# Optimization experiments

Measured on AMD Instinct MI355X. Metric: run time of the kernel, lower is better.

Reference implementation:

```python
import jax, jax.numpy as jnp
import numpy as np

B, S, DIM = 2, 2048, 2048
H, KV = 16, 8
HD = DIM // H          # 128 head_dim
N_REP = H // KV        # 2


def _rope(x, cos, sin):
    # x: (B,S,h,HD) with interleaved (real, imag) pairs along last dim
    xr = x[..., 0::2]                      # (B,S,h,HD/2)
    xi = x[..., 1::2]
    cos = cos[None, :, None, :]            # (1,S,1,HD/2)
    sin = sin[None, :, None, :]
    or_ = xr * cos - xi * sin
    oi_ = xr * sin + xi * cos
    return jnp.stack([or_, oi_], axis=-1).reshape(x.shape)


def setup_inputs() -> dict:
    key = jax.random.key(0)
    ks = jax.random.split(key, 5)
    x = jax.random.normal(ks[0], (B, S, DIM), dtype=jnp.float32)
    # RoPE tables: theta = 10000, half = HD/2
    inv_freq = 1.0 / (10000.0 ** (np.arange(0, HD, 2, dtype=np.float32) / HD))
    t = np.arange(S, dtype=np.float32)
    ang = np.outer(t, inv_freq)                           # (S, HD/2)
    freqs_cos = jnp.asarray(np.cos(ang), dtype=jnp.float32)
    freqs_sin = jnp.asarray(np.sin(ang), dtype=jnp.float32)
    sc = 0.02
    wq = jax.random.normal(ks[1], (DIM, H * HD), dtype=jnp.float32) * sc
    wk = jax.random.normal(ks[2], (DIM, KV * HD), dtype=jnp.float32) * sc
    wv = jax.random.normal(ks[3], (DIM, KV * HD), dtype=jnp.float32) * sc
    wo = jax.random.normal(ks[4], (DIM, DIM), dtype=jnp.float32) * sc
    return {"x": x, "freqs_cos": freqs_cos, "freqs_sin": freqs_sin,
            "wq": wq, "wk": wk, "wv": wv, "wo": wo}


def reference(x, freqs_cos, freqs_sin, wq, wk, wv, wo):
    b, s, _ = x.shape
    xq = (x @ wq).reshape(b, s, H, HD)
    xk = (x @ wk).reshape(b, s, KV, HD)
    xv = (x @ wv).reshape(b, s, KV, HD)
    xq = _rope(xq, freqs_cos, freqs_sin)
    xk = _rope(xk, freqs_cos, freqs_sin)
    # GQA: repeat kv heads n_rep times along head axis
    xk = jnp.repeat(xk, N_REP, axis=2)     # (b,s,H,HD)
    xv = jnp.repeat(xv, N_REP, axis=2)
    scores = jnp.einsum('bqhd,bkhd->bhqk', xq, xk) / jnp.sqrt(
        jnp.asarray(HD, dtype=x.dtype))
    mask = jnp.triu(jnp.full((s, s), -jnp.inf, dtype=x.dtype), k=1)
    attn = jax.nn.softmax(scores + mask[None, None, :, :], axis=-1)
    out = jnp.einsum('bhqk,bkhd->bqhd', attn, xv).reshape(b, s, DIM)
    return out @ wo
```

## Files before the change

### kernel.cpp

```cpp
#include <hip/hip_runtime.h>

typedef unsigned short u16;
typedef short bf16x8 __attribute__((ext_vector_type(8)));
typedef float f32x4 __attribute__((ext_vector_type(4)));
typedef float f32x16 __attribute__((ext_vector_type(16)));
typedef int i32x2 __attribute__((ext_vector_type(2)));
typedef unsigned int u32x4 __attribute__((ext_vector_type(4)));
typedef unsigned short u16x4 __attribute__((ext_vector_type(4)));
typedef unsigned short u16x8 __attribute__((ext_vector_type(8)));

#define S_LEN 2048
#define NHEAD 16
#define NKV 8
#define HD 128

__device__ __forceinline__ u16 f2bf(float f) {
  unsigned u = __builtin_bit_cast(unsigned, f);
  u = (u + 0x7FFFu + ((u >> 16) & 1u)) >> 16;
  return (u16)u;
}
__device__ __forceinline__ float bf2f(u16 h) {
  unsigned u = ((unsigned)h) << 16;
  return __builtin_bit_cast(float, u);
}

__device__ __forceinline__ void gl_lds16(const void* g, void* l) {
  __builtin_amdgcn_global_load_lds(
      (const __attribute__((address_space(1))) unsigned int*)g,
      (__attribute__((address_space(3))) unsigned int*)l, 16, 0, 0);
}

__device__ __forceinline__ unsigned cvtpk_bf16(float a, float b) {
  unsigned r;
  asm("v_cvt_pk_bf16_f32 %0, %1, %2" : "=v"(r) : "v"(a), "v"(b));
  return r;
}

__global__ __launch_bounds__(256) void conv_bf16(const float* __restrict__ in,
                                                 u16* __restrict__ out, int n4) {
  int i = blockIdx.x * 256 + threadIdx.x;
  if (i >= n4) return;
  f32x4 v = *(const f32x4*)(in + (size_t)i * 4);
  u16x4 o;
#pragma unroll
  for (int j = 0; j < 4; ++j) o[j] = f2bf(v[j]);
  *(u16x4*)(out + (size_t)i * 4) = o;
}

__global__ __launch_bounds__(256) void transpose_w4(
    const float* __restrict__ wq, const float* __restrict__ wk,
    const float* __restrict__ wv, const float* __restrict__ wo,
    u16* __restrict__ wcatT, u16* __restrict__ woT) {
  __shared__ float tile[64][65];
  int id = blockIdx.x;
  const float* in;
  u16* out;
  int N, roff, nx;
  if (id < 1024) {
    in = wq; out = wcatT; N = 2048; roff = 0; nx = 32;
  } else if (id < 1536) {
    in = wk; out = wcatT; N = 1024; roff = 2048; nx = 16; id -= 1024;
  } else if (id < 2048) {
    in = wv; out = wcatT; N = 1024; roff = 3072; nx = 16; id -= 1536;
  } else {
    in = wo; out = woT; N = 2048; roff = 0; nx = 32; id -= 2048;
  }
  int bx = id % nx;
  int by = id / nx;
  int k0 = by * 64, n0 = bx * 64;
  int tx = threadIdx.x & 63, ty = threadIdx.x >> 6;
#pragma unroll
  for (int p = 0; p < 16; ++p) {
    int r = p * 4 + ty;
    tile[r][tx] = in[(size_t)(k0 + r) * N + n0 + tx];
  }
  __syncthreads();
#pragma unroll
  for (int p = 0; p < 16; ++p) {
    int r = p * 4 + ty;
    out[(size_t)(roff + n0 + r) * 2048 + k0 + tx] = f2bf(tile[tx][r]);
  }
}

__global__ __launch_bounds__(256) void rope_qk(u16* __restrict__ q, u16* __restrict__ k,
                                               const float* __restrict__ fc,
                                               const float* __restrict__ fs) {
  const int QC = 2 * NHEAD * S_LEN * HD / 8;
  const int KC = 2 * NKV * S_LEN * HD / 8;
  int i = blockIdx.x * 256 + threadIdx.x;
  if (i >= QC + KC) return;
  u16* base;
  float scale;
  size_t e;
  if (i < QC) {
    base = q;
    e = (size_t)i * 8;
    scale = 0.12751744540368598f;
  } else {
    base = k;
    e = (size_t)(i - QC) * 8;
    scale = 1.0f;
  }
  int d8 = (int)(e & 127);
  int s = (int)((e >> 7) & (S_LEN - 1));
  int dp0 = d8 >> 1;
  u16x8 v = *(const u16x8*)(base + e);
  u16x8 o;
#pragma unroll
  for (int p = 0; p < 4; ++p) {
    float xr = bf2f(v[2 * p]), xi = bf2f(v[2 * p + 1]);
    float c = fc[s * 64 + dp0 + p], sn = fs[s * 64 + dp0 + p];
    o[2 * p] = f2bf((xr * c - xi * sn) * scale);
    o[2 * p + 1] = f2bf((xr * sn + xi * c) * scale);
  }
  *(u16x8*)(base + e) = o;
}

template <int EPI>
__global__ __launch_bounds__(512, 1) void gemm3r(
    const u16* __restrict__ A, const u16* __restrict__ Bt, float* __restrict__ Cf,
    u16* __restrict__ Qo, u16* __restrict__ Ko, u16* __restrict__ Vo, int N, int ntn) {
  constexpr int K = 2048, NT = K / 64;
  constexpr int BSZ = (128 + 256) * 64;
  __shared__ __align__(16) u16 lds[3][BSZ];

  const int t = threadIdx.x;
  const int l = t & 63, lh = l >> 4, ll = l & 15;
  const int w = t >> 6, wm = w >> 2, wn = w & 3;

  const int bid = blockIdx.x;
  const int swz = (bid & 7) * (gridDim.x >> 3) + (bid >> 3);
  const int tm = swz / ntn, tn = swz % ntn;

  const u16* Ab = A + (size_t)tm * 128 * K;
  const u16* Bb = Bt + (size_t)tn * 256 * K;

  const int sr = t >> 3;
  const int sc8 = ((t & 7) ^ (sr & 7)) * 8;

  f32x4 acc[4][4] = {};

  auto STAGE = [&](int tau) {
    const int kt = tau * 64;
    u16* buf = &lds[tau % 3][0];
#pragma unroll
    for (int c = 0; c < 2; ++c)
      gl_lds16(Ab + (size_t)(c * 64 + sr) * K + kt + sc8, buf + c * 4096 + t * 8);
#pragma unroll
    for (int c = 0; c < 4; ++c)
      gl_lds16(Bb + (size_t)(c * 64 + sr) * K + kt + sc8,
               buf + 8192 + c * 4096 + t * 8);
  };

  STAGE(0);
  STAGE(1);
  __builtin_amdgcn_s_waitcnt(0xF70 | 6);
  __builtin_amdgcn_s_barrier();
  asm volatile("" ::: "memory");

  for (int tt = 0; tt < NT; ++tt) {
    if (tt + 2 < NT) STAGE(tt + 2);
    const u16* bufA = &lds[tt % 3][0];
    const u16* bufB = bufA + 8192;
#pragma unroll
    for (int kk = 0; kk < 2; ++kk) {
      const int cb = ((kk * 4 + lh) ^ (ll & 7)) * 8;
      bf16x8 af[4], bv[4];
#pragma unroll
      for (int m = 0; m < 4; ++m)
        af[m] = *(const bf16x8*)(bufA + (wm * 64 + m * 16 + ll) * 64 + cb);
#pragma unroll
      for (int n = 0; n < 4; ++n)
        bv[n] = *(const bf16x8*)(bufB + (wn * 64 + n * 16 + ll) * 64 + cb);
      __builtin_amdgcn_s_setprio(1);
#pragma unroll
      for (int m = 0; m < 4; ++m)
#pragma unroll
        for (int n = 0; n < 4; ++n)
          acc[m][n] =
              __builtin_amdgcn_mfma_f32_16x16x32_bf16(af[m], bv[n], acc[m][n], 0, 0, 0);
      __builtin_amdgcn_s_setprio(0);
    }
    if (tt + 1 < NT) {
      if (tt + 2 < NT)
        __builtin_amdgcn_s_waitcnt(0xF70 | 6);
      else
        __builtin_amdgcn_s_waitcnt(0xF70);
      __builtin_amdgcn_s_barrier();
      asm volatile("" ::: "memory");
    }
  }

#pragma unroll
  for (int m = 0; m < 4; ++m)
#pragma unroll
    for (int n = 0; n < 4; ++n)
#pragma unroll
      for (int j = 0; j < 4; ++j) {
        int row = tm * 128 + wm * 64 + m * 16 + lh * 4 + j;
        int col = tn * 256 + wn * 64 + n * 16 + ll;
        if constexpr (EPI == 0) {
          Cf[(size_t)row * N + col] = acc[m][n][j];
        } else {
          int b = row >> 11, s = row & (S_LEN - 1);
          u16 val = f2bf(acc[m][n][j]);
          int d = col & 127;
          if (col < 2048) {
            int hh = col >> 7;
            Qo[(((size_t)b * NHEAD + hh) * S_LEN + s) * HD + d] = val;
          } else if (col < 3072) {
            int kh = (col >> 7) & 7;
            Ko[(((size_t)b * NKV + kh) * S_LEN + s) * HD + d] = val;
          } else {
            int kh = (col >> 7) & 7;
            Vo[(((size_t)b * NKV + kh) * S_LEN + s) * HD + d] = val;
          }
        }
      }
}

__global__ __launch_bounds__(256) void transpose_v(const u16* __restrict__ V,
                                                   u16* __restrict__ Vt) {
  __shared__ u16 tile[64][72];
  int id = blockIdx.x;
  int bkv = id >> 6;
  int dt = (id >> 5) & 1;
  int st = id & 31;
  const u16* Vb = V + (size_t)bkv * S_LEN * HD;
  u16* Vo = Vt + (size_t)bkv * HD * S_LEN;
  int r = threadIdx.x >> 3, c8 = (threadIdx.x & 7) * 8;
#pragma unroll
  for (int it = 0; it < 2; ++it) {
    int rr = it * 32 + r;
    *(u16x8*)(&tile[rr][c8]) =
        *(const u16x8*)(Vb + (size_t)(st * 64 + rr) * HD + dt * 64 + c8);
  }
  __syncthreads();
#pragma unroll
  for (int it = 0; it < 2; ++it) {
    int rr = it * 32 + r;
    u16x8 o;
#pragma unroll
    for (int j = 0; j < 8; ++j) o[j] = tile[c8 + j][rr];
    *(u16x8*)(Vo + (size_t)(dt * 64 + rr) * S_LEN + st * 64 + c8) = o;
  }
}

__global__ __launch_bounds__(256, 2) void attn_fwd(const u16* __restrict__ Q,
                                                   const u16* __restrict__ Kh,
                                                   const u16* __restrict__ Vt,
                                                   u16* __restrict__ O) {
  __shared__ __align__(16) u16 KS[2][64 * 128];
  __shared__ __align__(16) u16 VS[2][128 * 64];

  const int t = threadIdx.x;
  const int l = t & 63, hi = l >> 5, ll = l & 31;
  const int wq = t >> 6;

  const int bid = blockIdx.x;
  const int qt = 15 - (bid >> 5);
  const int bh = bid & 31;
  const int b = bh >> 4, h = bh & 15;
  const int bkv = b * NKV + (h >> 1);

  const u16* Qb = Q + (size_t)bh * S_LEN * HD;
  const u16* Kb = Kh + (size_t)bkv * S_LEN * HD;
  const u16* Vb = Vt + (size_t)bkv * HD * S_LEN;

  const int q0w = qt * 128 + wq * 32;
  const int qg = q0w + ll;

  bf16x8 qf[8];
#pragma unroll
  for (int c = 0; c < 8; ++c)
    qf[c] = *(const bf16x8*)(Qb + (size_t)qg * HD + c * 16 + hi * 8);

  const int krow = t >> 4, kslot = t & 15;
  const int vrow = t >> 3, vslot = t & 7;
  u16x8 krg[4], vrg[4];

  auto loadKV = [&](int tile) {
    const int kv0 = tile * 64;
#pragma unroll
    for (int c = 0; c < 4; ++c) {
      int r = c * 16 + krow;
      int sg = (kslot & 8) | ((kslot & 7) ^ (r & 7));
      krg[c] = *(const u16x8*)(Kb + (size_t)(kv0 + r) * HD + sg * 8);
    }
#pragma unroll
    for (int c = 0; c < 4; ++c) {
      int d = c * 32 + vrow;
      int sg = vslot ^ (d & 7);
      vrg[c] = *(const u16x8*)(Vb + (size_t)d * S_LEN + kv0 + sg * 8);
    }
  };
  auto storeKV = [&](int bi) {
#pragma unroll
    for (int c = 0; c < 4; ++c)
      *(u16x8*)(&KS[bi][(c * 16 + krow) * 128 + kslot * 8]) = krg[c];
#pragma unroll
    for (int c = 0; c < 4; ++c)
      *(u16x8*)(&VS[bi][(c * 32 + vrow) * 64 + vslot * 8]) = vrg[c];
  };

  f32x16 accO[4] = {};
  float m = -1e30f, lsum = 0.f;

  const int nt = 2 * qt + 2;
  loadKV(0);
  storeKV(0);
  __syncthreads();

  for (int tt = 0; tt < nt; ++tt) {
    const int kv0 = tt * 64;
    const bool actn = (tt + 1 < nt);
    if (actn) loadKV(tt + 1);

    if (kv0 <= q0w + 31) {
      const u16* ks = &KS[tt & 1][0];
      const u16* vs = &VS[tt & 1][0];

      f32x16 st[2] = {};
      __builtin_amdgcn_s_setprio(1);
#pragma unroll
      for (int c = 0; c < 8; ++c) {
        int slot = 2 * c + hi;
        int eff = (slot & 8) | ((slot & 7) ^ (ll & 7));
        bf16x8 kf0 = *(const bf16x8*)(ks + (size_t)ll * 128 + eff * 8);
        st[0] = __builtin_amdgcn_mfma_f32_32x32x16_bf16(kf0, qf[c], st[0], 0, 0, 0);
        bf16x8 kf1 = *(const bf16x8*)(ks + (size_t)(32 + ll) * 128 + eff * 8);
        st[1] = __builtin_amdgcn_mfma_f32_32x32x16_bf16(kf1, qf[c], st[1], 0, 0, 0);
      }
      __builtin_amdgcn_s_setprio(0);

      if (kv0 + 63 > q0w) {
#pragma unroll
        for (int f = 0; f < 2; ++f)
#pragma unroll
          for (int r = 0; r < 16; ++r) {
            int kvg = kv0 + f * 32 + (r & 3) + 8 * (r >> 2) + 4 * hi;
            if (kvg > qg) st[f][r] = -1e30f;
          }
      }

      float a[16];
#pragma unroll
      for (int i = 0; i < 16; ++i) a[i] = fmaxf(st[0][i], st[1][i]);
#pragma unroll
      for (int s = 8; s >= 1; s >>= 1)
#pragma unroll
        for (int i = 0; i < 8; ++i)
          if (i < s) a[i] = fmaxf(a[i], a[i + s]);
      float pmax = fmaxf(a[0], __shfl_xor(a[0], 32));

      if (tt == 0) {
        m = pmax;
      } else if (!__all(pmax <= m + 8.0f)) {
        float mnew = fmaxf(m, pmax);
        float corr = __builtin_amdgcn_exp2f(m - mnew);
        m = mnew;
        lsum *= corr;
        int ci = __builtin_bit_cast(int, corr);
#pragma unroll
        for (int reg = 0; reg < 16; ++reg) {
          int row = (reg & 3) + 8 * (reg >> 2) + 4 * hi;
          float cq = __builtin_bit_cast(
              float, __builtin_amdgcn_ds_bpermute(row << 2, ci));
#pragma unroll
          for (int dblk = 0; dblk < 4; ++dblk) accO[dblk][reg] *= cq;
        }
      }

#pragma unroll
      for (int f = 0; f < 2; ++f)
#pragma unroll
        for (int r = 0; r < 16; ++r)
          st[f][r] = __builtin_amdgcn_exp2f(st[f][r] - m);
      float s1[16];
#pragma unroll
      for (int i = 0; i < 16; ++i) s1[i] = st[0][i] + st[1][i];
#pragma unroll
      for (int s = 8; s >= 1; s >>= 1)
#pragma unroll
        for (int i = 0; i < 8; ++i)
          if (i < s) s1[i] += s1[i + s];
      lsum += s1[0];

      unsigned pk[8][2];
#pragma unroll
      for (int bg = 0; bg < 8; ++bg)
#pragma unroll
        for (int ap = 0; ap < 2; ++ap)
          pk[bg][ap] = cvtpk_bf16(st[bg >> 2][(bg & 3) * 4 + 2 * ap],
                                  st[bg >> 2][(bg & 3) * 4 + 2 * ap + 1]);

      __builtin_amdgcn_s_setprio(1);
#pragma unroll
      for (int kc = 0; kc < 4; ++kc) {
        i32x2 sa = __builtin_amdgcn_permlane32_swap(
            (int)pk[2 * kc][0], (int)pk[2 * kc + 1][0], false, false);
        i32x2 sb = __builtin_amdgcn_permlane32_swap(
            (int)pk[2 * kc][1], (int)pk[2 * kc + 1][1], false, false);
        union {
          unsigned u[4];
          bf16x8 v;
        } pa;
        pa.u[0] = (unsigned)sa[0];
        pa.u[1] = (unsigned)sb[0];
        pa.u[2] = (unsigned)sa[1];
        pa.u[3] = (unsigned)sb[1];
        int eff = (2 * kc + hi) ^ (ll & 7);
#pragma unroll
        for (int dblk = 0; dblk < 4; ++dblk) {
          bf16x8 vf = *(const bf16x8*)(vs + (size_t)(dblk * 32 + ll) * 64 + eff * 8);
          accO[dblk] =
              __builtin_amdgcn_mfma_f32_32x32x16_bf16(pa.v, vf, accO[dblk], 0, 0, 0);
        }
      }
      __builtin_amdgcn_s_setprio(0);
    }

    __syncthreads();
    if (actn) storeKV((tt + 1) & 1);
    __syncthreads();
  }

  lsum += __shfl_xor(lsum, 32);
  float linv = 1.0f / lsum;
  int li = __builtin_bit_cast(int, linv);
  float inv[16];
#pragma unroll
  for (int reg = 0; reg < 16; ++reg) {
    int row = (reg & 3) + 8 * (reg >> 2) + 4 * hi;
    inv[reg] = __builtin_bit_cast(float, __builtin_amdgcn_ds_bpermute(row << 2, li));
  }
#pragma unroll
  for (int dblk = 0; dblk < 4; ++dblk)
#pragma unroll
    for (int reg = 0; reg < 16; ++reg) {
      int row = (reg & 3) + 8 * (reg >> 2) + 4 * hi;
      O[(size_t)(b * S_LEN + q0w + row) * 2048 + h * HD + dblk * 32 + ll] =
          f2bf(accO[dblk][reg] * inv[reg]);
    }
}

extern "C" void kernel_launch(void* const* d_in, const int* in_sizes, int n_in,
                              void* d_out, int out_size, void* d_ws, size_t ws_size,
                              hipStream_t stream) {
  (void)in_sizes;
  (void)n_in;
  (void)out_size;
  (void)ws_size;
  const float* x = (const float*)d_in[0];
  const float* fc = (const float*)d_in[1];
  const float* fs = (const float*)d_in[2];
  const float* wq = (const float*)d_in[3];
  const float* wk = (const float*)d_in[4];
  const float* wv = (const float*)d_in[5];
  const float* wo = (const float*)d_in[6];
  float* out = (float*)d_out;

  char* ws = (char*)d_ws;
  u16* wcatT = (u16*)ws;
  u16* vtb = (u16*)ws;
  u16* woT = (u16*)(ws + 16777216);
  u16* xo = (u16*)(ws + 25165824);
  u16* qb = (u16*)(ws + 41943040);
  u16* kb = (u16*)(ws + 58720256);
  u16* vb = (u16*)(ws + 67108864);

  conv_bf16<<<8192, 256, 0, stream>>>(x, xo, 2097152);
  transpose_w4<<<3072, 256, 0, stream>>>(wq, wk, wv, wo, wcatT, woT);

  gemm3r<1><<<512, 512, 0, stream>>>(xo, wcatT, nullptr, qb, kb, vb, 4096, 16);
  transpose_v<<<1024, 256, 0, stream>>>(vb, vtb);
  rope_qk<<<6144, 256, 0, stream>>>(qb, kb, fc, fs);
  attn_fwd<<<512, 256, 0, stream>>>(qb, kb, vtb, xo);
  gemm3r<0><<<256, 512, 0, stream>>>(xo, woT, out, nullptr, nullptr, nullptr, 2048, 8);
}
```

Baseline: 212.3 us.

## Enlarge GEMM tiles to 256x256 with 4-stage K=32 LDS pipeline

Replaces the 128x256 GEMM tile and its 3-stage K=64 pipeline with a 256x256 tile that streams K in 32-wide slices through a 4-deep LDS ring. A and B rows share one combined swizzled buffer, and each wave now holds 8x4 accumulators. This raises arithmetic intensity per byte loaded and halves the grid. The cost is fewer blocks: 256 and 128 on a machine with 256 CUs, which leaves part of the GPU idle for the output projection. It also raises register pressure, and the launch bound now asks for 2 blocks per CU.

```diff
diff --git a/kernel.cpp b/kernel.cpp
--- a/kernel.cpp
+++ b/kernel.cpp
@@ -117,12 +117,11 @@
 }
 
 template <int EPI>
-__global__ __launch_bounds__(512, 1) void gemm3r(
+__global__ __launch_bounds__(512, 2) void gemm8p(
     const u16* __restrict__ A, const u16* __restrict__ Bt, float* __restrict__ Cf,
     u16* __restrict__ Qo, u16* __restrict__ Ko, u16* __restrict__ Vo, int N, int ntn) {
-  constexpr int K = 2048, NT = K / 64;
-  constexpr int BSZ = (128 + 256) * 64;
-  __shared__ __align__(16) u16 lds[3][BSZ];
+  constexpr int K = 2048, NH = K / 32;
+  __shared__ __align__(16) u16 lds[4][256 * 64];
 
   const int t = threadIdx.x;
   const int l = t & 63, lh = l >> 4, ll = l & 15;
@@ -132,78 +131,85 @@
   const int swz = (bid & 7) * (gridDim.x >> 3) + (bid >> 3);
   const int tm = swz / ntn, tn = swz % ntn;
 
-  const u16* Ab = A + (size_t)tm * 128 * K;
+  const u16* Ab = A + (size_t)tm * 256 * K;
   const u16* Bb = Bt + (size_t)tn * 256 * K;
 
-  const int sr = t >> 3;
-  const int sc8 = ((t & 7) ^ (sr & 7)) * 8;
-
-  f32x4 acc[4][4] = {};
-
-  auto STAGE = [&](int tau) {
-    const int kt = tau * 64;
-    u16* buf = &lds[tau % 3][0];
-#pragma unroll
-    for (int c = 0; c < 2; ++c)
-      gl_lds16(Ab + (size_t)(c * 64 + sr) * K + kt + sc8, buf + c * 4096 + t * 8);
+  const int srow = t >> 3;
+  const int sphys = t & 7;
+  const int slog = sphys ^ (srow & 7);
+  const u16* sbase = (slog < 4) ? Ab : Bb;
+  const int scol = (slog & 3) * 8;
+
+  f32x4 acc[8][4] = {};
+
+  auto STAGE = [&](int H) {
+    u16* buf = &lds[H & 3][0];
+    const u16* sp = sbase + (size_t)srow * K + H * 32 + scol;
 #pragma unroll
     for (int c = 0; c < 4; ++c)
-      gl_lds16(Bb + (size_t)(c * 64 + sr) * K + kt + sc8,
-               buf + 8192 + c * 4096 + t * 8);
+      gl_lds16(sp + (size_t)c * 64 * K, buf + c * 4096 + t * 8);
+  };
+
+  auto BODY = [&](int H) {
+    const u16* buf = &lds[H & 3][0];
+    bf16x8 af[8], bv[4];
+#pragma unroll
+    for (int i = 0; i < 8; ++i) {
+      int row = wm * 128 + i * 16 + ll;
+      af[i] = *(const bf16x8*)(buf + row * 64 + (lh ^ (ll & 7)) * 8);
+    }
+#pragma unroll
+    for (int n = 0; n < 4; ++n) {
+      int row = wn * 64 + n * 16 + ll;
+      bv[n] = *(const bf16x8*)(buf + row * 64 + ((4 + lh) ^ (ll & 7)) * 8);
+    }
+    __builtin_amdgcn_s_setprio(1);
+#pragma unroll
+    for (int i = 0; i < 8; ++i)
+#pragma unroll
+      for (int n = 0; n < 4; ++n)
+        acc[i][n] =
+            __builtin_amdgcn_mfma_f32_16x16x32_bf16(af[i], bv[n], acc[i][n], 0, 0, 0);
+    __builtin_amdgcn_s_setprio(0);
   };
 
   STAGE(0);
   STAGE(1);
-  __builtin_amdgcn_s_waitcnt(0xF70 | 6);
+  STAGE(2);
+  __builtin_amdgcn_s_waitcnt(0xF70 | 8);
   __builtin_amdgcn_s_barrier();
   asm volatile("" ::: "memory");
 
-  for (int tt = 0; tt < NT; ++tt) {
-    if (tt + 2 < NT) STAGE(tt + 2);
-    const u16* bufA = &lds[tt % 3][0];
-    const u16* bufB = bufA + 8192;
-#pragma unroll
-    for (int kk = 0; kk < 2; ++kk) {
-      const int cb = ((kk * 4 + lh) ^ (ll & 7)) * 8;
-      bf16x8 af[4], bv[4];
-#pragma unroll
-      for (int m = 0; m < 4; ++m)
-        af[m] = *(const bf16x8*)(bufA + (wm * 64 + m * 16 + ll) * 64 + cb);
-#pragma unroll
-      for (int n = 0; n < 4; ++n)
-        bv[n] = *(const bf16x8*)(bufB + (wn * 64 + n * 16 + ll) * 64 + cb);
-      __builtin_amdgcn_s_setprio(1);
-#pragma unroll
-      for (int m = 0; m < 4; ++m)
-#pragma unroll
-        for (int n = 0; n < 4; ++n)
-          acc[m][n] =
-              __builtin_amdgcn_mfma_f32_16x16x32_bf16(af[m], bv[n], acc[m][n], 0, 0, 0);
-      __builtin_amdgcn_s_setprio(0);
-    }
-    if (tt + 1 < NT) {
-      if (tt + 2 < NT)
-        __builtin_amdgcn_s_waitcnt(0xF70 | 6);
-      else
-        __builtin_amdgcn_s_waitcnt(0xF70);
-      __builtin_amdgcn_s_barrier();
-      asm volatile("" ::: "memory");
-    }
-  }
-
-#pragma unroll
-  for (int m = 0; m < 4; ++m)
+  for (int H = 0; H < NH - 3; ++H) {
+    STAGE(H + 3);
+    BODY(H);
+    __builtin_amdgcn_s_waitcnt(0xF70 | 8);
+    __builtin_amdgcn_s_barrier();
+    asm volatile("" ::: "memory");
+  }
+  BODY(NH - 3);
+  __builtin_amdgcn_s_waitcnt(0xF70 | 4);
+  __builtin_amdgcn_s_barrier();
+  asm volatile("" ::: "memory");
+  BODY(NH - 2);
+  __builtin_amdgcn_s_waitcnt(0xF70);
+  __builtin_amdgcn_s_barrier();
+  asm volatile("" ::: "memory");
+  BODY(NH - 1);
+
+#pragma unroll
+  for (int i = 0; i < 8; ++i)
 #pragma unroll
     for (int n = 0; n < 4; ++n)
 #pragma unroll
       for (int j = 0; j < 4; ++j) {
-        int row = tm * 128 + wm * 64 + m * 16 + lh * 4 + j;
+        int row = tm * 256 + wm * 128 + i * 16 + lh * 4 + j;
         int col = tn * 256 + wn * 64 + n * 16 + ll;
         if constexpr (EPI == 0) {
-          Cf[(size_t)row * N + col] = acc[m][n][j];
+          Cf[(size_t)row * N + col] = acc[i][n][j];
         } else {
           int b = row >> 11, s = row & (S_LEN - 1);
-          u16 val = f2bf(acc[m][n][j]);
+          u16 val = f2bf(acc[i][n][j]);
           int d = col & 127;
           if (col < 2048) {
             int hh = col >> 7;
@@ -472,9 +478,9 @@
   conv_bf16<<<8192, 256, 0, stream>>>(x, xo, 2097152);
   transpose_w4<<<3072, 256, 0, stream>>>(wq, wk, wv, wo, wcatT, woT);
 
-  gemm3r<1><<<512, 512, 0, stream>>>(xo, wcatT, nullptr, qb, kb, vb, 4096, 16);
+  gemm8p<1><<<256, 512, 0, stream>>>(xo, wcatT, nullptr, qb, kb, vb, 4096, 16);
   transpose_v<<<1024, 256, 0, stream>>>(vb, vtb);
   rope_qk<<<6144, 256, 0, stream>>>(qb, kb, fc, fs);
   attn_fwd<<<512, 256, 0, stream>>>(qb, kb, vtb, xo);
-  gemm3r<0><<<256, 512, 0, stream>>>(xo, woT, out, nullptr, nullptr, nullptr, 2048, 8);
-}
+  gemm8p<0><<<128, 512, 0, stream>>>(xo, woT, out, nullptr, nullptr, nullptr, 2048, 8);
+}
```

Result: slower. 223.8 us (+5.4%).

## Replace 128x256 GEMM tile with 128x128 tile, 256 threads, BK=32

Applied to the files above, without the earlier changes.

Both GEMMs move from a 128x256 output tile with 512 threads and a K-step of 64 to a 128x128 tile with 256 threads and a K-step of 32. The A and B tiles are interleaved in one shared LDS buffer, with a per-thread XOR swizzle that picks A or B. The grid is doubled so more blocks are in flight, and the smaller LDS and launch-bounds footprint allows more than one block per CU. In exchange, each loaded byte is reused less and there are twice as many barriers per unit of K.

```diff
diff --git a/kernel.cpp b/kernel.cpp
--- a/kernel.cpp
+++ b/kernel.cpp
@@ -117,73 +117,74 @@
 }
 
 template <int EPI>
-__global__ __launch_bounds__(512, 1) void gemm3r(
+__global__ __launch_bounds__(256) void gemm128(
     const u16* __restrict__ A, const u16* __restrict__ Bt, float* __restrict__ Cf,
     u16* __restrict__ Qo, u16* __restrict__ Ko, u16* __restrict__ Vo, int N, int ntn) {
-  constexpr int K = 2048, NT = K / 64;
-  constexpr int BSZ = (128 + 256) * 64;
-  __shared__ __align__(16) u16 lds[3][BSZ];
+  constexpr int K = 2048, NT = K / 32;
+  __shared__ __align__(16) u16 lds[3][128 * 64];
 
   const int t = threadIdx.x;
   const int l = t & 63, lh = l >> 4, ll = l & 15;
-  const int w = t >> 6, wm = w >> 2, wn = w & 3;
+  const int w = t >> 6, wm = w >> 1, wn = w & 1;
 
   const int bid = blockIdx.x;
   const int swz = (bid & 7) * (gridDim.x >> 3) + (bid >> 3);
   const int tm = swz / ntn, tn = swz % ntn;
 
   const u16* Ab = A + (size_t)tm * 128 * K;
-  const u16* Bb = Bt + (size_t)tn * 256 * K;
-
-  const int sr = t >> 3;
-  const int sc8 = ((t & 7) ^ (sr & 7)) * 8;
+  const u16* Bb = Bt + (size_t)tn * 128 * K;
+
+  const int srow = t >> 3;
+  const int sphys = t & 7;
+  const int slog = sphys ^ (srow & 7);
+  const u16* sbase = (slog < 4) ? Ab : Bb;
+  const int scol = (slog & 3) * 8;
 
   f32x4 acc[4][4] = {};
 
-  auto STAGE = [&](int tau) {
-    const int kt = tau * 64;
-    u16* buf = &lds[tau % 3][0];
-#pragma unroll
-    for (int c = 0; c < 2; ++c)
-      gl_lds16(Ab + (size_t)(c * 64 + sr) * K + kt + sc8, buf + c * 4096 + t * 8);
+  auto STAGE = [&](int tt) {
+    u16* buf = &lds[tt % 3][0];
+    const u16* sp = sbase + (size_t)srow * K + tt * 32 + scol;
 #pragma unroll
     for (int c = 0; c < 4; ++c)
-      gl_lds16(Bb + (size_t)(c * 64 + sr) * K + kt + sc8,
-               buf + 8192 + c * 4096 + t * 8);
+      gl_lds16(sp + (size_t)c * 32 * K, buf + c * 2048 + t * 8);
+  };
+
+  auto BODY = [&](int tt) {
+    const u16* buf = &lds[tt % 3][0];
+    bf16x8 af[4], bv[4];
+#pragma unroll
+    for (int m = 0; m < 4; ++m) {
+      int row = wm * 64 + m * 16 + ll;
+      af[m] = *(const bf16x8*)(buf + row * 64 + (lh ^ (ll & 7)) * 8);
+    }
+#pragma unroll
+    for (int n = 0; n < 4; ++n) {
+      int row = wn * 64 + n * 16 + ll;
+      bv[n] = *(const bf16x8*)(buf + row * 64 + ((4 + lh) ^ (ll & 7)) * 8);
+    }
+    __builtin_amdgcn_s_setprio(1);
+#pragma unroll
+    for (int m = 0; m < 4; ++m)
+#pragma unroll
+      for (int n = 0; n < 4; ++n)
+        acc[m][n] =
+            __builtin_amdgcn_mfma_f32_16x16x32_bf16(af[m], bv[n], acc[m][n], 0, 0, 0);
+    __builtin_amdgcn_s_setprio(0);
   };
 
   STAGE(0);
   STAGE(1);
-  __builtin_amdgcn_s_waitcnt(0xF70 | 6);
+  __builtin_amdgcn_s_waitcnt(0xF70 | 4);
   __builtin_amdgcn_s_barrier();
   asm volatile("" ::: "memory");
 
   for (int tt = 0; tt < NT; ++tt) {
     if (tt + 2 < NT) STAGE(tt + 2);
-    const u16* bufA = &lds[tt % 3][0];
-    const u16* bufB = bufA + 8192;
-#pragma unroll
-    for (int kk = 0; kk < 2; ++kk) {
-      const int cb = ((kk * 4 + lh) ^ (ll & 7)) * 8;
-      bf16x8 af[4], bv[4];
-#pragma unroll
-      for (int m = 0; m < 4; ++m)
-        af[m] = *(const bf16x8*)(bufA + (wm * 64 + m * 16 + ll) * 64 + cb);
-#pragma unroll
-      for (int n = 0; n < 4; ++n)
-        bv[n] = *(const bf16x8*)(bufB + (wn * 64 + n * 16 + ll) * 64 + cb);
-      __builtin_amdgcn_s_setprio(1);
-#pragma unroll
-      for (int m = 0; m < 4; ++m)
-#pragma unroll
-        for (int n = 0; n < 4; ++n)
-          acc[m][n] =
-              __builtin_amdgcn_mfma_f32_16x16x32_bf16(af[m], bv[n], acc[m][n], 0, 0, 0);
-      __builtin_amdgcn_s_setprio(0);
-    }
+    BODY(tt);
     if (tt + 1 < NT) {
       if (tt + 2 < NT)
-        __builtin_amdgcn_s_waitcnt(0xF70 | 6);
+        __builtin_amdgcn_s_waitcnt(0xF70 | 4);
       else
         __builtin_amdgcn_s_waitcnt(0xF70);
       __builtin_amdgcn_s_barrier();
@@ -198,7 +199,7 @@
 #pragma unroll
       for (int j = 0; j < 4; ++j) {
         int row = tm * 128 + wm * 64 + m * 16 + lh * 4 + j;
-        int col = tn * 256 + wn * 64 + n * 16 + ll;
+        int col = tn * 128 + wn * 64 + n * 16 + ll;
         if constexpr (EPI == 0) {
           Cf[(size_t)row * N + col] = acc[m][n][j];
         } else {
@@ -472,9 +473,9 @@
   conv_bf16<<<8192, 256, 0, stream>>>(x, xo, 2097152);
   transpose_w4<<<3072, 256, 0, stream>>>(wq, wk, wv, wo, wcatT, woT);
 
-  gemm3r<1><<<512, 512, 0, stream>>>(xo, wcatT, nullptr, qb, kb, vb, 4096, 16);
+  gemm128<1><<<1024, 256, 0, stream>>>(xo, wcatT, nullptr, qb, kb, vb, 4096, 32);
   transpose_v<<<1024, 256, 0, stream>>>(vb, vtb);
   rope_qk<<<6144, 256, 0, stream>>>(qb, kb, fc, fs);
   attn_fwd<<<512, 256, 0, stream>>>(qb, kb, vtb, xo);
-  gemm3r<0><<<256, 512, 0, stream>>>(xo, woT, out, nullptr, nullptr, nullptr, 2048, 8);
-}
+  gemm128<0><<<512, 256, 0, stream>>>(xo, woT, out, nullptr, nullptr, nullptr, 2048, 16);
+}
```

Result: slower. 247.2 us (+16.5%).

## Fuse RoPE and V transpose into QKV GEMM epilogue; split-K output GEMM

Applied to the files above, without the earlier changes.

Applies RoPE (with the query scale) inside the QKV GEMM epilogue, using a lane shuffle to fetch the pair partner. The V tile is transposed through LDS and written straight into the Vt layout, which removes the separate rope_qk and transpose_v kernels and their extra global round trips. The output projection is split along K into two halves over 512 blocks and accumulated with fp32 atomics into an output buffer zeroed beforehand. This fills more CUs, at the cost of atomic traffic, an extra zeroing kernel and order-dependent float summation.

```diff
diff --git a/kernel.cpp b/kernel.cpp
--- a/kernel.cpp
+++ b/kernel.cpp
@@ -45,6 +45,12 @@
 #pragma unroll
   for (int j = 0; j < 4; ++j) o[j] = f2bf(v[j]);
   *(u16x4*)(out + (size_t)i * 4) = o;
+}
+
+__global__ __launch_bounds__(256) void zero_f32(float* __restrict__ p, int n4) {
+  int i = blockIdx.x * 256 + threadIdx.x;
+  if (i >= n4) return;
+  *(f32x4*)(p + (size_t)i * 4) = f32x4{0.f, 0.f, 0.f, 0.f};
 }
 
 __global__ __launch_bounds__(256) void transpose_w4(
@@ -82,45 +88,13 @@
   }
 }
 
-__global__ __launch_bounds__(256) void rope_qk(u16* __restrict__ q, u16* __restrict__ k,
-                                               const float* __restrict__ fc,
-                                               const float* __restrict__ fs) {
-  const int QC = 2 * NHEAD * S_LEN * HD / 8;
-  const int KC = 2 * NKV * S_LEN * HD / 8;
-  int i = blockIdx.x * 256 + threadIdx.x;
-  if (i >= QC + KC) return;
-  u16* base;
-  float scale;
-  size_t e;
-  if (i < QC) {
-    base = q;
-    e = (size_t)i * 8;
-    scale = 0.12751744540368598f;
-  } else {
-    base = k;
-    e = (size_t)(i - QC) * 8;
-    scale = 1.0f;
-  }
-  int d8 = (int)(e & 127);
-  int s = (int)((e >> 7) & (S_LEN - 1));
-  int dp0 = d8 >> 1;
-  u16x8 v = *(const u16x8*)(base + e);
-  u16x8 o;
-#pragma unroll
-  for (int p = 0; p < 4; ++p) {
-    float xr = bf2f(v[2 * p]), xi = bf2f(v[2 * p + 1]);
-    float c = fc[s * 64 + dp0 + p], sn = fs[s * 64 + dp0 + p];
-    o[2 * p] = f2bf((xr * c - xi * sn) * scale);
-    o[2 * p + 1] = f2bf((xr * sn + xi * c) * scale);
-  }
-  *(u16x8*)(base + e) = o;
-}
-
 template <int EPI>
 __global__ __launch_bounds__(512, 1) void gemm3r(
     const u16* __restrict__ A, const u16* __restrict__ Bt, float* __restrict__ Cf,
-    u16* __restrict__ Qo, u16* __restrict__ Ko, u16* __restrict__ Vo, int N, int ntn) {
-  constexpr int K = 2048, NT = K / 64;
+    u16* __restrict__ Qo, u16* __restrict__ Ko, u16* __restrict__ Vt,
+    const float* __restrict__ fc, const float* __restrict__ fs, int N, int ntn) {
+  constexpr int K = 2048;
+  constexpr int NT = (EPI == 1) ? 32 : 16;
   constexpr int BSZ = (128 + 256) * 64;
   __shared__ __align__(16) u16 lds[3][BSZ];
 
@@ -129,11 +103,14 @@
   const int w = t >> 6, wm = w >> 2, wn = w & 3;
 
   const int bid = blockIdx.x;
-  const int swz = (bid & 7) * (gridDim.x >> 3) + (bid >> 3);
+  const int inner = (EPI == 1) ? bid : (bid & 255);
+  const int ngrid = (EPI == 1) ? 512 : 256;
+  const int koff = (EPI == 1) ? 0 : ((bid >> 8) * 1024);
+  const int swz = (inner & 7) * (ngrid >> 3) + (inner >> 3);
   const int tm = swz / ntn, tn = swz % ntn;
 
-  const u16* Ab = A + (size_t)tm * 128 * K;
-  const u16* Bb = Bt + (size_t)tn * 256 * K;
+  const u16* Ab = A + (size_t)tm * 128 * K + koff;
+  const u16* Bb = Bt + (size_t)tn * 256 * K + koff;
 
   const int sr = t >> 3;
   const int sc8 = ((t & 7) ^ (sr & 7)) * 8;
@@ -191,58 +168,68 @@
     }
   }
 
-#pragma unroll
-  for (int m = 0; m < 4; ++m)
-#pragma unroll
-    for (int n = 0; n < 4; ++n)
-#pragma unroll
-      for (int j = 0; j < 4; ++j) {
-        int row = tm * 128 + wm * 64 + m * 16 + lh * 4 + j;
-        int col = tn * 256 + wn * 64 + n * 16 + ll;
-        if constexpr (EPI == 0) {
-          Cf[(size_t)row * N + col] = acc[m][n][j];
-        } else {
-          int b = row >> 11, s = row & (S_LEN - 1);
-          u16 val = f2bf(acc[m][n][j]);
-          int d = col & 127;
-          if (col < 2048) {
-            int hh = col >> 7;
-            Qo[(((size_t)b * NHEAD + hh) * S_LEN + s) * HD + d] = val;
-          } else if (col < 3072) {
-            int kh = (col >> 7) & 7;
-            Ko[(((size_t)b * NKV + kh) * S_LEN + s) * HD + d] = val;
-          } else {
-            int kh = (col >> 7) & 7;
-            Vo[(((size_t)b * NKV + kh) * S_LEN + s) * HD + d] = val;
+  if constexpr (EPI == 0) {
+#pragma unroll
+    for (int m = 0; m < 4; ++m)
+#pragma unroll
+      for (int n = 0; n < 4; ++n)
+#pragma unroll
+        for (int j = 0; j < 4; ++j) {
+          int row = tm * 128 + wm * 64 + m * 16 + lh * 4 + j;
+          int col = tn * 256 + wn * 64 + n * 16 + ll;
+          atomicAdd(&Cf[(size_t)row * N + col], acc[m][n][j]);
+        }
+  } else {
+    if (tn < 12) {
+      const float qsc = 0.12751744540368598f;
+#pragma unroll
+      for (int m = 0; m < 4; ++m)
+#pragma unroll
+        for (int n = 0; n < 4; ++n)
+#pragma unroll
+          for (int j = 0; j < 4; ++j) {
+            int row = tm * 128 + wm * 64 + m * 16 + lh * 4 + j;
+            int col = tn * 256 + wn * 64 + n * 16 + ll;
+            int s = row & (S_LEN - 1), d = col & 127;
+            float v = acc[m][n][j];
+            float p = __shfl_xor(v, 1);
+            int d2 = d >> 1;
+            float c = fc[s * 64 + d2], sn = fs[s * 64 + d2];
+            float r = (d & 1) ? (p * sn + v * c) : (v * c - p * sn);
+            int b = row >> 11;
+            if (tn < 8) {
+              Qo[(((size_t)b * NHEAD + (col >> 7)) * S_LEN + s) * HD + d] =
+                  f2bf(r * qsc);
+            } else {
+              Ko[(((size_t)b * NKV + ((col >> 7) & 7)) * S_LEN + s) * HD + d] =
+                  f2bf(r);
+            }
           }
-        }
-      }
-}
-
-__global__ __launch_bounds__(256) void transpose_v(const u16* __restrict__ V,
-                                                   u16* __restrict__ Vt) {
-  __shared__ u16 tile[64][72];
-  int id = blockIdx.x;
-  int bkv = id >> 6;
-  int dt = (id >> 5) & 1;
-  int st = id & 31;
-  const u16* Vb = V + (size_t)bkv * S_LEN * HD;
-  u16* Vo = Vt + (size_t)bkv * HD * S_LEN;
-  int r = threadIdx.x >> 3, c8 = (threadIdx.x & 7) * 8;
-#pragma unroll
-  for (int it = 0; it < 2; ++it) {
-    int rr = it * 32 + r;
-    *(u16x8*)(&tile[rr][c8]) =
-        *(const u16x8*)(Vb + (size_t)(st * 64 + rr) * HD + dt * 64 + c8);
-  }
-  __syncthreads();
-#pragma unroll
-  for (int it = 0; it < 2; ++it) {
-    int rr = it * 32 + r;
-    u16x8 o;
-#pragma unroll
-    for (int j = 0; j < 8; ++j) o[j] = tile[c8 + j][rr];
-    *(u16x8*)(Vo + (size_t)(dt * 64 + rr) * S_LEN + st * 64 + c8) = o;
+    } else {
+      __syncthreads();
+      u16* vt = (u16*)&lds[0][0];
+#pragma unroll
+      for (int m = 0; m < 4; ++m)
+#pragma unroll
+        for (int n = 0; n < 4; ++n)
+#pragma unroll
+          for (int j = 0; j < 4; ++j) {
+            int sl = wm * 64 + m * 16 + lh * 4 + j;
+            int dcol = wn * 64 + n * 16 + ll;
+            vt[dcol * 136 + sl] = f2bf(acc[m][n][j]);
+          }
+      __syncthreads();
+      const int dcol = t >> 1, sh = (t & 1) * 64;
+      const int d = dcol & 127;
+      const int b = (tm * 128) >> 11;
+      const int s0 = (tm * 128) & (S_LEN - 1);
+      const int bkv = b * NKV + (tn - 12) * 2 + (dcol >> 7);
+      u16* dst = Vt + ((size_t)bkv * HD + d) * S_LEN + s0 + sh;
+      const u16* src = vt + dcol * 136 + sh;
+#pragma unroll
+      for (int c = 0; c < 8; ++c)
+        *(u16x8*)(dst + c * 8) = *(const u16x8*)(src + c * 8);
+    }
   }
 }
 
@@ -462,19 +449,19 @@
 
   char* ws = (char*)d_ws;
   u16* wcatT = (u16*)ws;
-  u16* vtb = (u16*)ws;
   u16* woT = (u16*)(ws + 16777216);
   u16* xo = (u16*)(ws + 25165824);
   u16* qb = (u16*)(ws + 41943040);
   u16* kb = (u16*)(ws + 58720256);
-  u16* vb = (u16*)(ws + 67108864);
+  u16* vtb = (u16*)(ws + 67108864);
 
   conv_bf16<<<8192, 256, 0, stream>>>(x, xo, 2097152);
   transpose_w4<<<3072, 256, 0, stream>>>(wq, wk, wv, wo, wcatT, woT);
 
-  gemm3r<1><<<512, 512, 0, stream>>>(xo, wcatT, nullptr, qb, kb, vb, 4096, 16);
-  transpose_v<<<1024, 256, 0, stream>>>(vb, vtb);
-  rope_qk<<<6144, 256, 0, stream>>>(qb, kb, fc, fs);
+  gemm3r<1><<<512, 512, 0, stream>>>(xo, wcatT, nullptr, qb, kb, vtb, fc, fs, 4096,
+                                     16);
   attn_fwd<<<512, 256, 0, stream>>>(qb, kb, vtb, xo);
-  gemm3r<0><<<256, 512, 0, stream>>>(xo, woT, out, nullptr, nullptr, nullptr, 2048, 8);
-}
+  zero_f32<<<8192, 256, 0, stream>>>(out, 2097152);
+  gemm3r<0><<<512, 512, 0, stream>>>(xo, woT, out, nullptr, nullptr, nullptr, nullptr,
+                                     nullptr, 2048, 8);
+}
```

Measured after the change: 243.9 us. 14.9% more time.
